# Kernel tuning notes

Measured on AMD Instinct MI355X. Metric: run time of the kernel, lower is better.

## Reference

```python
import jax, jax.numpy as jnp
import numpy as np

DIM = 1024
NUM_HEADS = 16
HEAD_DIM = DIM // NUM_HEADS
MLP_HIDDEN = 4 * DIM
TAU = 2.0
EPS = 1e-6
ALPHA_INIT = 0.01


def _xavier(key, out_f, in_f):
    limit = float(np.sqrt(6.0 / (in_f + out_f)))
    return jax.random.uniform(key, (out_f, in_f), jnp.float32, -limit, limit)


def setup_inputs() -> dict:
    key = jax.random.key(0)
    ks = jax.random.split(key, 10)
    B, Lq, Lkv = 4, 512, 2048
    return {
        "q_tokens": jax.random.normal(ks[0], (B, Lq, DIM), jnp.float32),
        "kv_tokens": jax.random.normal(ks[1], (B, Lkv, DIM), jnp.float32),
        "q_ln_w": jnp.ones((DIM,), jnp.float32),
        "q_ln_b": jnp.zeros((DIM,), jnp.float32),
        "kv_ln_w": jnp.ones((DIM,), jnp.float32),
        "kv_ln_b": jnp.zeros((DIM,), jnp.float32),
        "mlp_ln_w": jnp.ones((DIM,), jnp.float32),
        "mlp_ln_b": jnp.zeros((DIM,), jnp.float32),
        "Wq": _xavier(ks[2], DIM, DIM),
        "Wk": _xavier(ks[3], DIM, DIM),
        "Wv": _xavier(ks[4], DIM, DIM),
        "Wo": _xavier(ks[5], DIM, DIM),
        "bo": jnp.zeros((DIM,), jnp.float32),
        "fc1_w": _xavier(ks[6], MLP_HIDDEN, DIM),
        "fc1_b": jnp.zeros((MLP_HIDDEN,), jnp.float32),
        "fc2_w": _xavier(ks[7], DIM, MLP_HIDDEN),
        "fc2_b": jnp.zeros((DIM,), jnp.float32),
        "alpha_attn": jnp.full((1,), ALPHA_INIT, jnp.float32),
        "alpha_mlp": jnp.full((1,), ALPHA_INIT, jnp.float32),
    }


def _ln(x, w, b):
    mu = jnp.mean(x, axis=-1, keepdims=True)
    var = jnp.var(x, axis=-1, keepdims=True)
    return (x - mu) * jax.lax.rsqrt(var + EPS) * w + b


def _l2norm(x):
    # matches torch F.normalize: x / max(||x||, eps)
    n = jnp.sqrt(jnp.sum(x * x, axis=-1, keepdims=True))
    return x / jnp.maximum(n, EPS)


def reference(q_tokens, kv_tokens, q_ln_w, q_ln_b, kv_ln_w, kv_ln_b,
              mlp_ln_w, mlp_ln_b, Wq, Wk, Wv, Wo, bo,
              fc1_w, fc1_b, fc2_w, fc2_b, alpha_attn, alpha_mlp):
    B, Lq, D = q_tokens.shape
    q = _ln(q_tokens, q_ln_w, q_ln_b) @ Wq.T  # [B,Lq,D]
    kvn = _ln(kv_tokens, kv_ln_w, kv_ln_b)
    k = kvn @ Wk.T
    v = kvn @ Wv.T
    # split heads -> [B,H,L,hd]
    q = q.reshape(B, Lq, NUM_HEADS, HEAD_DIM)
    k = k.reshape(B, -1, NUM_HEADS, HEAD_DIM)
    v = v.reshape(B, -1, NUM_HEADS, HEAD_DIM)
    q = _l2norm(q)
    k = _l2norm(k)
    scores = jnp.einsum('bqhd,bkhd->bhqk', q, k) / TAU
    attn = jax.nn.softmax(scores, axis=-1)
    ctx = jnp.einsum('bhqk,bkhd->bqhd', attn, v).reshape(B, Lq, D)
    ctx = ctx @ Wo.T + bo
    out = q_tokens + alpha_attn * ctx
    h = _ln(out, mlp_ln_w, mlp_ln_b)
    h = jax.nn.gelu(h @ fc1_w.T + fc1_b, approximate=False)
    h = h @ fc2_w.T + fc2_b
    return out + alpha_mlp * h
```

## Files before the change

kernel.cpp:

```cpp
#include <hip/hip_runtime.h>


typedef __attribute__((ext_vector_type(8))) short short8_t;
typedef __attribute__((ext_vector_type(4))) short short4_t;
typedef __attribute__((ext_vector_type(4))) float f32x4_t;

#define WSCALE 16.0f
#define OSC (1.0f / 16.0f)

__device__ __forceinline__ float b2f(short s) {
    union { float f; unsigned u; } c;
    c.u = ((unsigned)(unsigned short)s) << 16;
    return c.f;
}
__device__ __forceinline__ short f2b(float f) {
    union { float f; unsigned u; } c;
    c.f = f;
    unsigned u = c.u;
    unsigned r = (u + 0x7FFFu + ((u >> 16) & 1u)) >> 16;
    return (short)r;
}
__device__ __forceinline__ unsigned cvt_pk_bf16(float lo, float hi) {
    unsigned r;
    asm("v_cvt_pk_bf16_f32 %0, %1, %2" : "=v"(r) : "v"(lo), "v"(hi));
    return r;
}
__device__ __forceinline__ unsigned f2f8_pk4(float a, float b, float c, float d) {
    int lo = __builtin_amdgcn_cvt_pk_fp8_f32(a, b, 0, false);
    return (unsigned)__builtin_amdgcn_cvt_pk_fp8_f32(c, d, lo, true);
}
__device__ __forceinline__ unsigned char f2f8(float a) {
    return (unsigned char)(__builtin_amdgcn_cvt_pk_fp8_f32(a, a, 0, false) & 0xff);
}

__device__ __forceinline__ void gload16(const void* g, void* l) {
    __builtin_amdgcn_global_load_lds(
        (const __attribute__((address_space(1))) void*)g,
        (__attribute__((address_space(3))) void*)l, 16, 0, 0);
}

template <int OUT8>
__device__ __forceinline__ void ln_row(
    const float* __restrict__ x, const float* __restrict__ w,
    const float* __restrict__ bia, void* __restrict__ y,
    int row, int tid, float* red)
{
    const float4 t = *(const float4*)(x + (size_t)row * 1024 + tid * 4);
    float v[4] = {t.x, t.y, t.z, t.w};
    float s = v[0] + v[1] + v[2] + v[3];
    float s2 = v[0]*v[0] + v[1]*v[1] + v[2]*v[2] + v[3]*v[3];
    #pragma unroll
    for (int off = 1; off < 64; off <<= 1) {
        s  += __shfl_xor(s, off);
        s2 += __shfl_xor(s2, off);
    }
    const int wave = tid >> 6, lane = tid & 63;
    if (lane == 0) { red[wave] = s; red[4 + wave] = s2; }
    __syncthreads();
    s  = red[0] + red[1] + red[2] + red[3];
    s2 = red[4] + red[5] + red[6] + red[7];
    const float mu  = s * (1.0f / 1024.0f);
    const float var = s2 * (1.0f / 1024.0f) - mu * mu;
    const float rstd = rsqrtf(var + 1e-6f);
    const float4 wv = *(const float4*)(w + tid * 4);
    const float4 bv = *(const float4*)(bia + tid * 4);
    const float o0 = (v[0] - mu) * rstd * wv.x + bv.x;
    const float o1 = (v[1] - mu) * rstd * wv.y + bv.y;
    const float o2 = (v[2] - mu) * rstd * wv.z + bv.z;
    const float o3 = (v[3] - mu) * rstd * wv.w + bv.w;
    if (OUT8) {
        ((unsigned*)y)[(size_t)row * 256 + tid] = f2f8_pk4(o0, o1, o2, o3);
    } else {
        short4 o;
        o.x = f2b(o0); o.y = f2b(o1); o.z = f2b(o2); o.w = f2b(o3);
        *(short4*)((short*)y + (size_t)row * 1024 + tid * 4) = o;
    }
}

__global__ __launch_bounds__(256) void prep_kernel(
    const float* __restrict__ qt, const float* __restrict__ kvt,
    const float* __restrict__ qlw, const float* __restrict__ qlb,
    const float* __restrict__ klw, const float* __restrict__ klb,
    short* __restrict__ qn, unsigned char* __restrict__ kvn8,
    const float* __restrict__ Wq, const float* __restrict__ Wo,
    const float* __restrict__ Wk, const float* __restrict__ Wv,
    const float* __restrict__ fc1w, const float* __restrict__ fc2w,
    short* __restrict__ Wq_b, short* __restrict__ Wo_b,
    unsigned char* __restrict__ Wkv8,
    unsigned char* __restrict__ fc1_8, unsigned char* __restrict__ fc2_8)
{
    __shared__ float red[8];
    const int bid = blockIdx.x, tid = threadIdx.x;
    if (bid < 2048) {
        ln_row<0>(qt, qlw, qlb, qn, bid, tid, red);
    } else if (bid < 10240) {
        ln_row<1>(kvt, klw, klb, kvn8, bid - 2048, tid, red);
    } else {
        int f = (bid - 10240) * 256 + tid;
        if (f < 524288) {
            const float* src = (f < 262144) ? Wq : Wo;
            short* dst = (f < 262144) ? Wq_b : Wo_b;
            const int off = f & 262143;
            const float4 v = ((const float4*)src)[off];
            short4 o;
            o.x = f2b(v.x); o.y = f2b(v.y); o.z = f2b(v.z); o.w = f2b(v.w);
            ((short4*)dst)[off] = o;
        } else {
            const float* src; unsigned* dst; int off;
            if (f < 1048576) {
                off = f - 524288;
                src = (off < 262144) ? Wk : Wv;
                dst = (unsigned*)Wkv8;
                if (off >= 262144) { src = Wv; }
                const int so = (off < 262144) ? off : off - 262144;
                const float4 v = ((const float4*)src)[so];
                dst[off] = f2f8_pk4(v.x * WSCALE, v.y * WSCALE,
                                    v.z * WSCALE, v.w * WSCALE);
                return;
            } else if (f < 2097152) {
                off = f - 1048576; src = fc1w; dst = (unsigned*)fc1_8;
            } else {
                off = f - 2097152; src = fc2w; dst = (unsigned*)fc2_8;
            }
            const float4 v = ((const float4*)src)[off];
            dst[off] = f2f8_pk4(v.x * WSCALE, v.y * WSCALE,
                                v.z * WSCALE, v.w * WSCALE);
        }
    }
}

__global__ __launch_bounds__(256) void ln8_kernel(
    const float* __restrict__ x, const float* __restrict__ w,
    const float* __restrict__ bia, unsigned char* __restrict__ y)
{
    __shared__ float red[8];
    ln_row<1>(x, w, bia, y, blockIdx.x, threadIdx.x, red);
}

template <int EPI, int BM>
__global__ __launch_bounds__(256) void gemm_bt_kernel(
    const short* __restrict__ A, const short* __restrict__ W,
    int M, int N, int Ks, int Kst,
    const float* __restrict__ bias,
    const float* __restrict__ resF,
    const float* __restrict__ alpha,
    short* __restrict__ out16,
    float* __restrict__ outF)
{
    constexpr int MI = (BM + 31) / 32;
    __shared__ __attribute__((aligned(16))) short As[2][BM * 64];
    __shared__ __attribute__((aligned(16))) short Bs[2][128 * 64];
    const int bm = blockIdx.y * BM, bn = blockIdx.x * 128;
    const int tid = threadIdx.x;
    const int wave = tid >> 6, lane = tid & 63;
    const int wm = (wave >> 1) * (BM / 2), wn = (wave & 1) * 64;
    const int l15 = lane & 15, quad = lane >> 4;
    const int l7 = l15 & 7;

    f32x4_t acc[MI][4];
    #pragma unroll
    for (int mi = 0; mi < MI; ++mi)
        #pragma unroll
        for (int ni = 0; ni < 4; ++ni)
            acc[mi][ni] = (f32x4_t){0.f, 0.f, 0.f, 0.f};

    auto stage = [&](int buf, int k0) {
        #pragma unroll
        for (int c = 0; c < BM / 32; ++c) {
            const int o = c * 4096 + tid * 16;
            const int row = o >> 7;
            const int g = ((o >> 4) & 7) ^ (row & 7);
            gload16(A + (size_t)(bm + row) * Kst + k0 + g * 8,
                    (char*)As[buf] + c * 4096 + wave * 1024);
        }
        #pragma unroll
        for (int c = 0; c < 4; ++c) {
            const int o = c * 4096 + tid * 16;
            const int row = o >> 7;
            const int g = ((o >> 4) & 7) ^ (row & 7);
            gload16(W + (size_t)(bn + row) * Kst + k0 + g * 8,
                    (char*)Bs[buf] + c * 4096 + wave * 1024);
        }
    };

    const int nIter = Ks >> 6;
    stage(0, 0);
    for (int it = 0; it < nIter; ++it) {
        const int buf = it & 1;
        __syncthreads();
        if (it + 1 < nIter) stage(buf ^ 1, (it + 1) * 64);
        #pragma unroll
        for (int h = 0; h < 2; ++h) {
            const int fg = (((h << 2) | quad) ^ l7) * 8;
            short8_t af[MI], bf[4];
            #pragma unroll
            for (int mi = 0; mi < MI; ++mi)
                af[mi] = *(const short8_t*)&As[buf][(wm + mi * 16 + l15) * 64 + fg];
            #pragma unroll
            for (int ni = 0; ni < 4; ++ni)
                bf[ni] = *(const short8_t*)&Bs[buf][(wn + ni * 16 + l15) * 64 + fg];
            #pragma unroll
            for (int mi = 0; mi < MI; ++mi)
                #pragma unroll
                for (int ni = 0; ni < 4; ++ni)
                    acc[mi][ni] = __builtin_amdgcn_mfma_f32_16x16x32_bf16(
                        af[mi], bf[ni], acc[mi][ni], 0, 0, 0);
        }
    }

    if (EPI == 4) {
        #pragma unroll
        for (int mi = 0; mi < MI; ++mi)
            #pragma unroll
            for (int r = 0; r < 4; ++r) {
                float s = 0.f;
                #pragma unroll
                for (int ni = 0; ni < 4; ++ni) {
                    const float x = acc[mi][ni][r];
                    s += x * x;
                }
                s += __shfl_xor(s, 1); s += __shfl_xor(s, 2);
                s += __shfl_xor(s, 4); s += __shfl_xor(s, 8);
                const float sc = 1.0f / fmaxf(sqrtf(s), 1e-6f);
                #pragma unroll
                for (int ni = 0; ni < 4; ++ni) acc[mi][ni][r] *= sc;
            }
    }

    const float a = (EPI == 1) ? alpha[0] : 0.f;
    #pragma unroll
    for (int mi = 0; mi < MI; ++mi) {
        #pragma unroll
        for (int ni = 0; ni < 4; ++ni) {
            const int n = bn + wn + ni * 16 + l15;
            const float bb = (EPI == 1) ? bias[n] : 0.f;
            #pragma unroll
            for (int r = 0; r < 4; ++r) {
                const int m = bm + wm + mi * 16 + (quad << 2) + r;
                const float x = acc[mi][ni][r];
                if (EPI == 4) {
                    out16[(size_t)m * N + n] = f2b(x);
                } else {
                    const size_t idx = (size_t)m * N + n;
                    outF[idx] = resF[idx] + a * (x + bb);
                }
            }
        }
    }
}

__device__ __forceinline__ void kvproj_body(
    unsigned char* __restrict__ pool, int bx, int by, int tid,
    const unsigned char* __restrict__ A, const unsigned char* __restrict__ W,
    short* __restrict__ khd, short* __restrict__ vhd)
{
    constexpr int BM = 128, BK = 64, MI = 4, KS = 2;
    constexpr int N = 2048, Kst = 1024;
    auto AsBuf = [&](int b) { return pool + b * (BM * BK); };
    auto BsBuf = [&](int b) { return pool + 2 * BM * BK + b * (128 * BK); };
    const int bm = by * BM, bn = bx * 128;
    const int wave = tid >> 6, lane = tid & 63;
    const int wm = (wave >> 1) * (BM / 2), wn = (wave & 1) * 64;
    const int l15 = lane & 15, quad = lane >> 4;

    f32x4_t acc[MI][4];
    #pragma unroll
    for (int mi = 0; mi < MI; ++mi)
        #pragma unroll
        for (int ni = 0; ni < 4; ++ni)
            acc[mi][ni] = (f32x4_t){0.f, 0.f, 0.f, 0.f};

    auto stage = [&](int buf, int k0) {
        #pragma unroll
        for (int c = 0; c < 2; ++c) {
            const int o = c * 4096 + tid * 16;
            const int row = o >> 6;
            const int g = ((o >> 4) & 3) ^ ((row >> 1) & 3);
            gload16(A + (size_t)(bm + row) * Kst + k0 + g * 16,
                    (char*)AsBuf(buf) + c * 4096 + wave * 1024);
        }
        #pragma unroll
        for (int c = 0; c < 2; ++c) {
            const int o = c * 4096 + tid * 16;
            const int row = o >> 6;
            const int g = ((o >> 4) & 3) ^ ((row >> 1) & 3);
            gload16(W + (size_t)(bn + row) * Kst + k0 + g * 16,
                    (char*)BsBuf(buf) + c * 4096 + wave * 1024);
        }
    };

    stage(0, 0);
    for (int it = 0; it < 16; ++it) {
        const int buf = it & 1;
        __syncthreads();
        if (it + 1 < 16) stage(buf ^ 1, (it + 1) * BK);
        #pragma unroll
        for (int ks = 0; ks < KS; ++ks) {
            const int fo = ((((ks << 1) | (quad >> 1)) ^ ((l15 >> 1) & 3)) << 4) +
                           (quad & 1) * 8;
            long af[MI], bf[4];
            #pragma unroll
            for (int mi = 0; mi < MI; ++mi)
                af[mi] = *(const long*)(AsBuf(buf) + (wm + mi * 16 + l15) * BK + fo);
            #pragma unroll
            for (int ni = 0; ni < 4; ++ni)
                bf[ni] = *(const long*)(BsBuf(buf) + (wn + ni * 16 + l15) * BK + fo);
            #pragma unroll
            for (int mi = 0; mi < MI; ++mi)
                #pragma unroll
                for (int ni = 0; ni < 4; ++ni)
                    acc[mi][ni] = __builtin_amdgcn_mfma_f32_16x16x32_fp8_fp8(
                        af[mi], bf[ni], acc[mi][ni], 0, 0, 0);
        }
    }

    const bool isK = (bn < 1024);
    if (isK) {
        #pragma unroll
        for (int mi = 0; mi < MI; ++mi)
            #pragma unroll
            for (int r = 0; r < 4; ++r) {
                float s = 0.f;
                #pragma unroll
                for (int ni = 0; ni < 4; ++ni) {
                    const float x = acc[mi][ni][r];
                    s += x * x;
                }
                s += __shfl_xor(s, 1); s += __shfl_xor(s, 2);
                s += __shfl_xor(s, 4); s += __shfl_xor(s, 8);
                const float sc = 1.0f / fmaxf(sqrtf(s), 1e-6f);
                #pragma unroll
                for (int ni = 0; ni < 4; ++ni) acc[mi][ni][r] *= sc;
            }
    }
    __syncthreads();
    short* Ct = (short*)pool;
    constexpr int LDC = 136;
    if (isK) {
        #pragma unroll
        for (int mi = 0; mi < MI; ++mi)
            #pragma unroll
            for (int ni = 0; ni < 4; ++ni) {
                const int n = wn + ni * 16 + l15;
                #pragma unroll
                for (int r = 0; r < 4; ++r)
                    Ct[(wm + mi * 16 + (quad << 2) + r) * LDC + n] =
                        f2b(acc[mi][ni][r]);
            }
    } else {
        #pragma unroll
        for (int mi = 0; mi < MI; ++mi)
            #pragma unroll
            for (int ni = 0; ni < 4; ++ni) {
                short4 pk;
                pk.x = f2b(acc[mi][ni][0] * OSC);
                pk.y = f2b(acc[mi][ni][1] * OSC);
                pk.z = f2b(acc[mi][ni][2] * OSC);
                pk.w = f2b(acc[mi][ni][3] * OSC);
                *(short4*)&Ct[(wn + ni * 16 + l15) * LDC +
                              wm + mi * 16 + (quad << 2)] = pk;
            }
    }
    __syncthreads();
    const int b_ = bm >> 11;
    const int kv0 = bm & 2047;
    #pragma unroll
    for (int p = 0; p < 8; ++p) {
        const int idx = p * 256 + tid;
        const int row = idx >> 4, ch = idx & 15;
        const short8_t v = *(const short8_t*)&Ct[row * LDC + ch * 8];
        if (isK) {
            const int hh = (bn >> 6) + (ch >> 3);
            *(short8_t*)&khd[(size_t)((b_ * 16 + hh) * 2048 + kv0 + row) * 64 +
                             (ch & 7) * 8] = v;
        } else {
            const int nn = bn - 1024 + row;
            *(short8_t*)&vhd[(size_t)((b_ * 16 + (nn >> 6)) * 64 +
                             (nn & 63)) * 2048 + kv0 + ch * 8] = v;
        }
    }
}

__device__ __forceinline__ void qproj_body(
    unsigned char* __restrict__ pool, int bx, int by, int tid,
    const short* __restrict__ A, const short* __restrict__ W,
    short* __restrict__ out16)
{
    constexpr int BM = 32, N = 1024, Kst = 1024;
    short* As = (short*)pool;
    short* Bs = (short*)(pool + 8192);
    const int bm = by * BM, bn = bx * 128;
    const int wave = tid >> 6, lane = tid & 63;
    const int wm = (wave >> 1) * 16, wn = (wave & 1) * 64;
    const int l15 = lane & 15, quad = lane >> 4;
    const int l7 = l15 & 7;

    f32x4_t acc[4];
    #pragma unroll
    for (int ni = 0; ni < 4; ++ni) acc[ni] = (f32x4_t){0.f, 0.f, 0.f, 0.f};

    auto stage = [&](int buf, int k0) {
        {
            const int o = tid * 16;
            const int row = o >> 7;
            const int g = ((o >> 4) & 7) ^ (row & 7);
            gload16(A + (size_t)(bm + row) * Kst + k0 + g * 8,
                    (char*)As + buf * 4096 + wave * 1024);
        }
        #pragma unroll
        for (int c = 0; c < 4; ++c) {
            const int o = c * 4096 + tid * 16;
            const int row = o >> 7;
            const int g = ((o >> 4) & 7) ^ (row & 7);
            gload16(W + (size_t)(bn + row) * Kst + k0 + g * 8,
                    (char*)Bs + buf * 16384 + c * 4096 + wave * 1024);
        }
    };

    stage(0, 0);
    for (int it = 0; it < 16; ++it) {
        const int buf = it & 1;
        __syncthreads();
        if (it + 1 < 16) stage(buf ^ 1, (it + 1) * 64);
        #pragma unroll
        for (int h = 0; h < 2; ++h) {
            const int fg = (((h << 2) | quad) ^ l7) * 8;
            const short8_t af =
                *(const short8_t*)&As[buf * 2048 + (wm + l15) * 64 + fg];
            short8_t bf[4];
            #pragma unroll
            for (int ni = 0; ni < 4; ++ni)
                bf[ni] = *(const short8_t*)&Bs[buf * 8192 +
                                               (wn + ni * 16 + l15) * 64 + fg];
            #pragma unroll
            for (int ni = 0; ni < 4; ++ni)
                acc[ni] = __builtin_amdgcn_mfma_f32_16x16x32_bf16(
                    af, bf[ni], acc[ni], 0, 0, 0);
        }
    }

    #pragma unroll
    for (int r = 0; r < 4; ++r) {
        float s = 0.f;
        #pragma unroll
        for (int ni = 0; ni < 4; ++ni) {
            const float x = acc[ni][r];
            s += x * x;
        }
        s += __shfl_xor(s, 1); s += __shfl_xor(s, 2);
        s += __shfl_xor(s, 4); s += __shfl_xor(s, 8);
        const float sc = 1.0f / fmaxf(sqrtf(s), 1e-6f);
        #pragma unroll
        for (int ni = 0; ni < 4; ++ni) acc[ni][r] *= sc;
    }
    #pragma unroll
    for (int ni = 0; ni < 4; ++ni) {
        const int n = bn + wn + ni * 16 + l15;
        #pragma unroll
        for (int r = 0; r < 4; ++r) {
            const int m = bm + wm + (quad << 2) + r;
            out16[(size_t)m * N + n] = f2b(acc[ni][r]);
        }
    }
}

__global__ __launch_bounds__(256, 4) void qkv_kernel(
    const unsigned char* __restrict__ kvn8, const unsigned char* __restrict__ Wkv8,
    short* __restrict__ khd, short* __restrict__ vhd,
    const short* __restrict__ qn, const short* __restrict__ Wq_b,
    short* __restrict__ qbuf)
{
    __shared__ __attribute__((aligned(16))) unsigned char pool[40960];
    const int id = blockIdx.x;
    const int xcd = id & 7, slot = id >> 3;
    const int by = xcd * 8 + (slot & 7);
    const int bx = slot >> 3;
    const int tid = threadIdx.x;
    if (bx < 16) kvproj_body(pool, bx, by, tid, kvn8, Wkv8, khd, vhd);
    else         qproj_body(pool, bx - 16, by, tid, qn, Wq_b, qbuf);
}

template <int EPI, int BM, int BK>
__global__ __launch_bounds__(256, 4) void gemm_f8_kernel(
    const unsigned char* __restrict__ A, const unsigned char* __restrict__ W,
    int M, int N, int Ks, int Kst,
    const float* __restrict__ bias,
    unsigned char* __restrict__ out8,
    short* __restrict__ out16,
    float* __restrict__ outF)
{
    constexpr int MI = BM / 32;
    constexpr int KS = BK / 32;
    constexpr int STG = 2 * BM * BK + 2 * 128 * BK;
    constexpr int EPIB = (EPI == 2) ? BM * 144 : 0;
    constexpr int POOL = (STG > EPIB) ? STG : EPIB;
    __shared__ __attribute__((aligned(16))) unsigned char pool[POOL];
    auto AsBuf = [&](int b) { return pool + b * (BM * BK); };
    auto BsBuf = [&](int b) { return pool + 2 * BM * BK + b * (128 * BK); };
    const int bm = blockIdx.y * BM, bn = blockIdx.x * 128;
    const size_t kbase = (size_t)blockIdx.z * Ks;
    const int tid = threadIdx.x;
    const int wave = tid >> 6, lane = tid & 63;
    const int wm = (wave >> 1) * (BM / 2), wn = (wave & 1) * 64;
    const int l15 = lane & 15, quad = lane >> 4;
    const int l7 = l15 & 7;

    f32x4_t acc[MI][4];
    #pragma unroll
    for (int mi = 0; mi < MI; ++mi)
        #pragma unroll
        for (int ni = 0; ni < 4; ++ni)
            acc[mi][ni] = (f32x4_t){0.f, 0.f, 0.f, 0.f};

    auto stage = [&](int buf, int k0) {
        #pragma unroll
        for (int c = 0; c < BM * BK / 4096; ++c) {
            const int o = c * 4096 + tid * 16;
            const int row = o / BK;
            int g;
            if constexpr (BK == 128) g = ((o >> 4) & 7) ^ (row & 7);
            else                     g = ((o >> 4) & 3) ^ ((row >> 1) & 3);
            gload16(A + (size_t)(bm + row) * Kst + kbase + k0 + g * 16,
                    (char*)AsBuf(buf) + c * 4096 + wave * 1024);
        }
        #pragma unroll
        for (int c = 0; c < 128 * BK / 4096; ++c) {
            const int o = c * 4096 + tid * 16;
            const int row = o / BK;
            int g;
            if constexpr (BK == 128) g = ((o >> 4) & 7) ^ (row & 7);
            else                     g = ((o >> 4) & 3) ^ ((row >> 1) & 3);
            gload16(W + (size_t)(bn + row) * Kst + kbase + k0 + g * 16,
                    (char*)BsBuf(buf) + c * 4096 + wave * 1024);
        }
    };

    const int nIter = Ks / BK;
    stage(0, 0);
    for (int it = 0; it < nIter; ++it) {
        const int buf = it & 1;
        __syncthreads();
        if (it + 1 < nIter) stage(buf ^ 1, (it + 1) * BK);
        #pragma unroll
        for (int ks = 0; ks < KS; ++ks) {
            int fo;
            if constexpr (BK == 128)
                fo = ((((ks << 1) | (quad >> 1)) ^ l7) << 4) + (quad & 1) * 8;
            else
                fo = ((((ks << 1) | (quad >> 1)) ^ ((l15 >> 1) & 3)) << 4) +
                     (quad & 1) * 8;
            long af[MI], bf[4];
            #pragma unroll
            for (int mi = 0; mi < MI; ++mi)
                af[mi] = *(const long*)(AsBuf(buf) + (wm + mi * 16 + l15) * BK + fo);
            #pragma unroll
            for (int ni = 0; ni < 4; ++ni)
                bf[ni] = *(const long*)(BsBuf(buf) + (wn + ni * 16 + l15) * BK + fo);
            #pragma unroll
            for (int mi = 0; mi < MI; ++mi)
                #pragma unroll
                for (int ni = 0; ni < 4; ++ni)
                    acc[mi][ni] = __builtin_amdgcn_mfma_f32_16x16x32_fp8_fp8(
                        af[mi], bf[ni], acc[mi][ni], 0, 0, 0);
        }
    }

    if (EPI == 2) {
        __syncthreads();
        unsigned char* C8 = (unsigned char*)pool;
        constexpr int LDC8 = 144;
        #pragma unroll
        for (int mi = 0; mi < MI; ++mi)
            #pragma unroll
            for (int ni = 0; ni < 4; ++ni) {
                const int n = wn + ni * 16 + l15;
                const float bb = bias[bn + n];
                #pragma unroll
                for (int r = 0; r < 4; ++r) {
                    const float t = acc[mi][ni][r] * OSC + bb;
                    C8[(wm + mi * 16 + (quad << 2) + r) * LDC8 + n] =
                        f2f8(0.5f * t * (1.0f + erff(t * 0.70710678118f)));
                }
            }
        __syncthreads();
        #pragma unroll
        for (int p = 0; p < MI; ++p) {
            const int idx = p * 256 + tid;
            const int row = idx >> 3, ch = idx & 7;
            const f32x4_t v = *(const f32x4_t*)&C8[row * LDC8 + ch * 16];
            *(f32x4_t*)&out8[(size_t)(bm + row) * N + bn + ch * 16] = v;
        }
        return;
    }

    #pragma unroll
    for (int mi = 0; mi < MI; ++mi) {
        #pragma unroll
        for (int ni = 0; ni < 4; ++ni) {
            const int n = bn + wn + ni * 16 + l15;
            #pragma unroll
            for (int r = 0; r < 4; ++r) {
                const int m = bm + wm + mi * 16 + (quad << 2) + r;
                out16[(size_t)blockIdx.z * M * N + (size_t)m * N + n] =
                    f2b(acc[mi][ni][r]);
            }
        }
    }
}

__global__ __launch_bounds__(256) void reduce4_kernel(
    const short* __restrict__ parts, const float* __restrict__ resF,
    const float* __restrict__ bias, const float* __restrict__ alpha,
    float* __restrict__ out)
{
    const int i = blockIdx.x * 256 + threadIdx.x;
    const size_t MN4 = (size_t)2048 * 1024 / 4;
    const float a = alpha[0];
    const float4 b4 = ((const float4*)bias)[i & 255];
    const short4 p0 = ((const short4*)parts)[i];
    const short4 p1 = ((const short4*)parts)[MN4 + i];
    const short4 p2 = ((const short4*)parts)[2 * MN4 + i];
    const short4 p3 = ((const short4*)parts)[3 * MN4 + i];
    const float4 rv = ((const float4*)resF)[i];
    float4 o;
    o.x = rv.x + a * ((b2f(p0.x) + b2f(p1.x) + b2f(p2.x) + b2f(p3.x)) * OSC + b4.x);
    o.y = rv.y + a * ((b2f(p0.y) + b2f(p1.y) + b2f(p2.y) + b2f(p3.y)) * OSC + b4.y);
    o.z = rv.z + a * ((b2f(p0.z) + b2f(p1.z) + b2f(p2.z) + b2f(p3.z)) * OSC + b4.z);
    o.w = rv.w + a * ((b2f(p0.w) + b2f(p1.w) + b2f(p2.w) + b2f(p3.w)) * OSC + b4.w);
    ((float4*)out)[i] = o;
}

__global__ __launch_bounds__(256, 4) void attn_kernel(
    const short* __restrict__ q, const short* __restrict__ khd,
    const short* __restrict__ vhd, short* __restrict__ o0,
    short* __restrict__ o1, float* __restrict__ lpart)
{
    const int h  = blockIdx.x;
    const int b  = blockIdx.y;
    const int qt = blockIdx.z >> 1;
    const int sp = blockIdx.z & 1;
    const int tid = threadIdx.x;
    const int wave = tid >> 6, lane = tid & 63;
    const int l15 = lane & 15, quad = lane >> 4;
    const int q0 = qt * 64 + wave * 16;
    const int t0 = sp * 16;

    __shared__ __attribute__((aligned(16))) short Ks[2][4096];
    __shared__ __attribute__((aligned(16))) short Vs[2][4096];

    const short* qbase = q + (size_t)(b * 512 + q0 + l15) * 1024 + h * 64 + quad * 8;
    const short8_t aq0 = *(const short8_t*)(qbase);
    const short8_t aq1 = *(const short8_t*)(qbase + 32);

    const short* kbase = khd + (size_t)(b * 16 + h) * 2048 * 64;
    const short* vbase = vhd + (size_t)(b * 16 + h) * 64 * 2048;

    const int swz = l15 & 7;
    const int g0 = (quad ^ swz) * 8;
    const int g1 = ((quad ^ swz) ^ 4) * 8;

    auto stage = [&](int buf, int t) {
        #pragma unroll
        for (int c = 0; c < 2; ++c) {
            const int o = c * 4096 + tid * 16;
            const int row = o >> 7;
            const int g = ((o >> 4) & 7) ^ (row & 7);
            gload16(kbase + (size_t)(t * 64 + row) * 64 + g * 8,
                    (char*)Ks[buf] + c * 4096 + wave * 1024);
            gload16(vbase + (size_t)row * 2048 + t * 64 + g * 8,
                    (char*)Vs[buf] + c * 4096 + wave * 1024);
        }
    };

    const short4_t ones4 = {(short)0x3F80, (short)0x3F80,
                            (short)0x3F80, (short)0x3F80};

    f32x4_t oacc[4];
    #pragma unroll
    for (int u = 0; u < 4; ++u) oacc[u] = (f32x4_t){0.f, 0.f, 0.f, 0.f};
    f32x4_t lacc = (f32x4_t){0.f, 0.f, 0.f, 0.f};

    stage(0, t0);
    for (int tt = 0; tt < 16; ++tt) {
        const int buf = tt & 1;
        __syncthreads();
        if (tt + 1 < 16) stage(buf ^ 1, t0 + tt + 1);

        f32x4_t s[4];
        __builtin_amdgcn_s_setprio(1);
        #pragma unroll
        for (int ss = 0; ss < 4; ++ss) {
            const int R = ss * 16 + l15;
            const short8_t bk0 = *(const short8_t*)&Ks[buf][R * 64 + g0];
            const short8_t bk1 = *(const short8_t*)&Ks[buf][R * 64 + g1];
            f32x4_t a = (f32x4_t){0.f, 0.f, 0.f, 0.f};
            a = __builtin_amdgcn_mfma_f32_16x16x32_bf16(bk0, aq0, a, 0, 0, 0);
            a = __builtin_amdgcn_mfma_f32_16x16x32_bf16(bk1, aq1, a, 0, 0, 0);
            s[ss] = a;
        }
        __builtin_amdgcn_s_setprio(0);
        short4_t pa[4];
        #pragma unroll
        for (int ss = 0; ss < 4; ++ss) {
            const float p0 = __expf(s[ss][0] * 0.5f);
            const float p1 = __expf(s[ss][1] * 0.5f);
            const float p2 = __expf(s[ss][2] * 0.5f);
            const float p3 = __expf(s[ss][3] * 0.5f);
            union { unsigned w[2]; short4_t v; } u_;
            u_.w[0] = cvt_pk_bf16(p0, p1);
            u_.w[1] = cvt_pk_bf16(p2, p3);
            pa[ss] = u_.v;
        }
        __builtin_amdgcn_s_setprio(1);
        #pragma unroll
        for (int ss = 0; ss < 4; ++ss)
            lacc = __builtin_amdgcn_mfma_f32_16x16x16bf16_1k(
                pa[ss], ones4, lacc, 0, 0, 0);
        #pragma unroll
        for (int ss = 0; ss < 4; ++ss) {
            const int ch = (((ss * 2 + (quad >> 1)) ^ swz) << 3) + ((quad & 1) << 2);
            #pragma unroll
            for (int u = 0; u < 4; ++u) {
                const short4_t bv =
                    *(const short4_t*)&Vs[buf][(u * 16 + l15) * 64 + ch];
                oacc[u] = __builtin_amdgcn_mfma_f32_16x16x16bf16_1k(
                    pa[ss], bv, oacc[u], 0, 0, 0);
            }
        }
        __builtin_amdgcn_s_setprio(0);
    }

    short* ob = sp ? o1 : o0;
    float* lb = lpart + (size_t)sp * 2048 * 16;
    #pragma unroll
    for (int u = 0; u < 4; ++u)
        #pragma unroll
        for (int r = 0; r < 4; ++r)
            ob[(size_t)(b * 512 + q0 + quad * 4 + r) * 1024 + h * 64 + u * 16 + l15] =
                f2b(oacc[u][r]);
    if (l15 == 0) {
        #pragma unroll
        for (int r = 0; r < 4; ++r)
            lb[(size_t)(b * 512 + q0 + quad * 4 + r) * 16 + h] = lacc[r];
    }
}

__global__ __launch_bounds__(256) void attn_combine_kernel(
    const short* __restrict__ o0, const short* __restrict__ o1,
    const float* __restrict__ lpart, short* __restrict__ ctx)
{
    const int i = blockIdx.x * 256 + threadIdx.x;
    const int row = i >> 8;
    const int h = (i & 255) >> 4;
    const float l = lpart[row * 16 + h] + lpart[2048 * 16 + row * 16 + h];
    const float inv = 1.0f / l;
    const short4 a4 = ((const short4*)o0)[i];
    const short4 c4 = ((const short4*)o1)[i];
    short4 o;
    o.x = f2b((b2f(a4.x) + b2f(c4.x)) * inv);
    o.y = f2b((b2f(a4.y) + b2f(c4.y)) * inv);
    o.z = f2b((b2f(a4.z) + b2f(c4.z)) * inv);
    o.w = f2b((b2f(a4.w) + b2f(c4.w)) * inv);
    ((short4*)ctx)[i] = o;
}

extern "C" void kernel_launch(void* const* d_in, const int* in_sizes, int n_in,
                              void* d_out, int out_size, void* d_ws, size_t ws_size,
                              hipStream_t stream)
{
    const float* q_tokens  = (const float*)d_in[0];
    const float* kv_tokens = (const float*)d_in[1];
    const float* q_ln_w    = (const float*)d_in[2];
    const float* q_ln_b    = (const float*)d_in[3];
    const float* kv_ln_w   = (const float*)d_in[4];
    const float* kv_ln_b   = (const float*)d_in[5];
    const float* mlp_ln_w  = (const float*)d_in[6];
    const float* mlp_ln_b  = (const float*)d_in[7];
    const float* Wq        = (const float*)d_in[8];
    const float* Wk        = (const float*)d_in[9];
    const float* Wv        = (const float*)d_in[10];
    const float* Wo        = (const float*)d_in[11];
    const float* bo        = (const float*)d_in[12];
    const float* fc1_w     = (const float*)d_in[13];
    const float* fc1_b     = (const float*)d_in[14];
    const float* fc2_w     = (const float*)d_in[15];
    const float* fc2_b     = (const float*)d_in[16];
    const float* alpha_attn = (const float*)d_in[17];
    const float* alpha_mlp  = (const float*)d_in[18];

    char* ws = (char*)d_ws;
    const size_t MB = (size_t)1 << 20;
    short* khd    = (short*)(ws);
    short* vhd    = (short*)(ws + 16 * MB);
    short* parts  = (short*)(ws);
    unsigned char* kvn8 = (unsigned char*)(ws + 32 * MB);
    short* attn_o0 = (short*)(ws + 32 * MB);
    unsigned char* h1   = (unsigned char*)(ws + 32 * MB);
    short* qn     = (short*)(ws + 40 * MB);
    short* qbuf   = (short*)(ws + 44 * MB);
    short* ctx    = (short*)(ws + 48 * MB);
    float* aout   = (float*)(ws + 52 * MB);
    short* attn_o1 = (short*)(ws + 52 * MB);
    unsigned char* hn8 = (unsigned char*)(ws + 60 * MB);
    float* attn_l  = (float*)(ws + 60 * MB);
    short* Wq_b   = (short*)(ws + 62 * MB);
    short* Wo_b   = (short*)(ws + 64 * MB);
    unsigned char* Wkv8  = (unsigned char*)(ws + 66 * MB);
    unsigned char* fc1_8 = (unsigned char*)(ws + 68 * MB);
    unsigned char* fc2_8 = (unsigned char*)(ws + 72 * MB);

    prep_kernel<<<22528, 256, 0, stream>>>(
        q_tokens, kv_tokens, q_ln_w, q_ln_b, kv_ln_w, kv_ln_b, qn, kvn8,
        Wq, Wo, Wk, Wv, fc1_w, fc2_w,
        Wq_b, Wo_b, Wkv8, fc1_8, fc2_8);

    qkv_kernel<<<1536, 256, 0, stream>>>(
        kvn8, Wkv8, khd, vhd, qn, Wq_b, qbuf);

    attn_kernel<<<dim3(16, 4, 16), 256, 0, stream>>>(
        qbuf, khd, vhd, attn_o0, attn_o1, attn_l);
    attn_combine_kernel<<<2048, 256, 0, stream>>>(attn_o0, attn_o1, attn_l, ctx);

    gemm_bt_kernel<1, 32><<<dim3(8, 64), 256, 0, stream>>>(
        ctx, Wo_b, 2048, 1024, 1024, 1024, bo, q_tokens, alpha_attn, nullptr, aout);

    ln8_kernel<<<2048, 256, 0, stream>>>(aout, mlp_ln_w, mlp_ln_b, hn8);

    gemm_f8_kernel<2, 64, 64><<<dim3(32, 32), 256, 0, stream>>>(
        hn8, fc1_8, 2048, 4096, 1024, 1024, fc1_b, h1, nullptr, nullptr);

    gemm_f8_kernel<7, 64, 64><<<dim3(8, 32, 4), 256, 0, stream>>>(
        h1, fc2_8, 2048, 1024, 1024, 4096, nullptr, nullptr, parts, nullptr);
    reduce4_kernel<<<2048, 256, 0, stream>>>(parts, aout, fc2_b, alpha_mlp,
                                             (float*)d_out);
}
```

Before: 282.4 us.

## Switch FP8 GEMMs to MI355 scaled 16x16x128 MFMA with BK=128 tiles

```diff
diff --git a/kernel.cpp b/kernel.cpp
--- a/kernel.cpp
+++ b/kernel.cpp
@@ -4,9 +4,12 @@
 typedef __attribute__((ext_vector_type(8))) short short8_t;
 typedef __attribute__((ext_vector_type(4))) short short4_t;
 typedef __attribute__((ext_vector_type(4))) float f32x4_t;
+typedef __attribute__((ext_vector_type(8))) int int8v_t;
+typedef __attribute__((ext_vector_type(4))) int int4v_t;
 
 #define WSCALE 16.0f
 #define OSC (1.0f / 16.0f)
+#define SCL1 127
 
 __device__ __forceinline__ float b2f(short s) {
     union { float f; unsigned u; } c;
@@ -37,6 +40,15 @@
     __builtin_amdgcn_global_load_lds(
         (const __attribute__((address_space(1))) void*)g,
         (__attribute__((address_space(3))) void*)l, 16, 0, 0);
+}
+
+__device__ __forceinline__ int8v_t ld32(const unsigned char* base, int g0, int g1) {
+    const int4v_t lo = *(const int4v_t*)(base + g0);
+    const int4v_t hi = *(const int4v_t*)(base + g1);
+    int8v_t r;
+    r[0] = lo[0]; r[1] = lo[1]; r[2] = lo[2]; r[3] = lo[3];
+    r[4] = hi[0]; r[5] = hi[1]; r[6] = hi[2]; r[7] = hi[3];
+    return r;
 }
 
 template <int OUT8>
@@ -254,14 +266,15 @@
     const unsigned char* __restrict__ A, const unsigned char* __restrict__ W,
     short* __restrict__ khd, short* __restrict__ vhd)
 {
-    constexpr int BM = 128, BK = 64, MI = 4, KS = 2;
-    constexpr int N = 2048, Kst = 1024;
+    constexpr int BM = 128, BK = 128, MI = 4;
+    constexpr int Kst = 1024;
     auto AsBuf = [&](int b) { return pool + b * (BM * BK); };
     auto BsBuf = [&](int b) { return pool + 2 * BM * BK + b * (128 * BK); };
     const int bm = by * BM, bn = bx * 128;
     const int wave = tid >> 6, lane = tid & 63;
     const int wm = (wave >> 1) * (BM / 2), wn = (wave & 1) * 64;
     const int l15 = lane & 15, quad = lane >> 4;
+    const int l7 = l15 & 7;
 
     f32x4_t acc[MI][4];
     #pragma unroll
@@ -272,46 +285,44 @@
 
     auto stage = [&](int buf, int k0) {
         #pragma unroll
-        for (int c = 0; c < 2; ++c) {
+        for (int c = 0; c < 4; ++c) {
             const int o = c * 4096 + tid * 16;
-            const int row = o >> 6;
-            const int g = ((o >> 4) & 3) ^ ((row >> 1) & 3);
+            const int row = o >> 7;
+            const int g = ((o >> 4) & 7) ^ (row & 7);
             gload16(A + (size_t)(bm + row) * Kst + k0 + g * 16,
                     (char*)AsBuf(buf) + c * 4096 + wave * 1024);
         }
         #pragma unroll
-        for (int c = 0; c < 2; ++c) {
+        for (int c = 0; c < 4; ++c) {
             const int o = c * 4096 + tid * 16;
-            const int row = o >> 6;
-            const int g = ((o >> 4) & 3) ^ ((row >> 1) & 3);
+            const int row = o >> 7;
+            const int g = ((o >> 4) & 7) ^ (row & 7);
             gload16(W + (size_t)(bn + row) * Kst + k0 + g * 16,
                     (char*)BsBuf(buf) + c * 4096 + wave * 1024);
         }
     };
 
+    const int ga = ((quad << 1) ^ l7) << 4;
+    const int gb = (((quad << 1) | 1) ^ l7) << 4;
+
     stage(0, 0);
-    for (int it = 0; it < 16; ++it) {
+    for (int it = 0; it < 8; ++it) {
         const int buf = it & 1;
         __syncthreads();
-        if (it + 1 < 16) stage(buf ^ 1, (it + 1) * BK);
-        #pragma unroll
-        for (int ks = 0; ks < KS; ++ks) {
-            const int fo = ((((ks << 1) | (quad >> 1)) ^ ((l15 >> 1) & 3)) << 4) +
-                           (quad & 1) * 8;
-            long af[MI], bf[4];
-            #pragma unroll
-            for (int mi = 0; mi < MI; ++mi)
-                af[mi] = *(const long*)(AsBuf(buf) + (wm + mi * 16 + l15) * BK + fo);
+        if (it + 1 < 8) stage(buf ^ 1, (it + 1) * BK);
+        int8v_t af[MI], bf[4];
+        #pragma unroll
+        for (int mi = 0; mi < MI; ++mi)
+            af[mi] = ld32(AsBuf(buf) + (wm + mi * 16 + l15) * BK, ga, gb);
+        #pragma unroll
+        for (int ni = 0; ni < 4; ++ni)
+            bf[ni] = ld32(BsBuf(buf) + (wn + ni * 16 + l15) * BK, ga, gb);
+        #pragma unroll
+        for (int mi = 0; mi < MI; ++mi)
             #pragma unroll
             for (int ni = 0; ni < 4; ++ni)
-                bf[ni] = *(const long*)(BsBuf(buf) + (wn + ni * 16 + l15) * BK + fo);
-            #pragma unroll
-            for (int mi = 0; mi < MI; ++mi)
-                #pragma unroll
-                for (int ni = 0; ni < 4; ++ni)
-                    acc[mi][ni] = __builtin_amdgcn_mfma_f32_16x16x32_fp8_fp8(
-                        af[mi], bf[ni], acc[mi][ni], 0, 0, 0);
-        }
+                acc[mi][ni] = __builtin_amdgcn_mfma_scale_f32_16x16x128_f8f6f4(
+                    af[mi], bf[ni], acc[mi][ni], 0, 0, 0, SCL1, 0, SCL1);
     }
 
     const bool isK = (bn < 1024);
@@ -464,13 +475,13 @@
     }
 }
 
-__global__ __launch_bounds__(256, 4) void qkv_kernel(
+__global__ __launch_bounds__(256, 2) void qkv_kernel(
     const unsigned char* __restrict__ kvn8, const unsigned char* __restrict__ Wkv8,
     short* __restrict__ khd, short* __restrict__ vhd,
     const short* __restrict__ qn, const short* __restrict__ Wq_b,
     short* __restrict__ qbuf)
 {
-    __shared__ __attribute__((aligned(16))) unsigned char pool[40960];
+    __shared__ __attribute__((aligned(16))) unsigned char pool[65536];
     const int id = blockIdx.x;
     const int xcd = id & 7, slot = id >> 3;
     const int by = xcd * 8 + (slot & 7);
@@ -480,8 +491,8 @@
     else         qproj_body(pool, bx - 16, by, tid, qn, Wq_b, qbuf);
 }
 
-template <int EPI, int BM, int BK>
-__global__ __launch_bounds__(256, 4) void gemm_f8_kernel(
+template <int EPI, int BM>
+__global__ __launch_bounds__(256, 2) void gemm_f8_kernel(
     const unsigned char* __restrict__ A, const unsigned char* __restrict__ W,
     int M, int N, int Ks, int Kst,
     const float* __restrict__ bias,
@@ -490,7 +501,7 @@
     float* __restrict__ outF)
 {
     constexpr int MI = BM / 32;
-    constexpr int KS = BK / 32;
+    constexpr int BK = 128;
     constexpr int STG = 2 * BM * BK + 2 * 128 * BK;
     constexpr int EPIB = (EPI == 2) ? BM * 144 : 0;
     constexpr int POOL = (STG > EPIB) ? STG : EPIB;
@@ -516,53 +527,43 @@
         #pragma unroll
         for (int c = 0; c < BM * BK / 4096; ++c) {
             const int o = c * 4096 + tid * 16;
-            const int row = o / BK;
-            int g;
-            if constexpr (BK == 128) g = ((o >> 4) & 7) ^ (row & 7);
-            else                     g = ((o >> 4) & 3) ^ ((row >> 1) & 3);
+            const int row = o >> 7;
+            const int g = ((o >> 4) & 7) ^ (row & 7);
             gload16(A + (size_t)(bm + row) * Kst + kbase + k0 + g * 16,
                     (char*)AsBuf(buf) + c * 4096 + wave * 1024);
         }
         #pragma unroll
-        for (int c = 0; c < 128 * BK / 4096; ++c) {
+        for (int c = 0; c < 4; ++c) {
             const int o = c * 4096 + tid * 16;
-            const int row = o / BK;
-            int g;
-            if constexpr (BK == 128) g = ((o >> 4) & 7) ^ (row & 7);
-            else                     g = ((o >> 4) & 3) ^ ((row >> 1) & 3);
+            const int row = o >> 7;
+            const int g = ((o >> 4) & 7) ^ (row & 7);
             gload16(W + (size_t)(bn + row) * Kst + kbase + k0 + g * 16,
                     (char*)BsBuf(buf) + c * 4096 + wave * 1024);
         }
     };
 
-    const int nIter = Ks / BK;
+    const int ga = ((quad << 1) ^ l7) << 4;
+    const int gb = (((quad << 1) | 1) ^ l7) << 4;
+
+    const int nIter = Ks >> 7;
     stage(0, 0);
     for (int it = 0; it < nIter; ++it) {
         const int buf = it & 1;
         __syncthreads();
         if (it + 1 < nIter) stage(buf ^ 1, (it + 1) * BK);
-        #pragma unroll
-        for (int ks = 0; ks < KS; ++ks) {
-            int fo;
-            if constexpr (BK == 128)
-                fo = ((((ks << 1) | (quad >> 1)) ^ l7) << 4) + (quad & 1) * 8;
-            else
-                fo = ((((ks << 1) | (quad >> 1)) ^ ((l15 >> 1) & 3)) << 4) +
-                     (quad & 1) * 8;
-            long af[MI], bf[4];
-            #pragma unroll
-            for (int mi = 0; mi < MI; ++mi)
-                af[mi] = *(const long*)(AsBuf(buf) + (wm + mi * 16 + l15) * BK + fo);
+        int8v_t af[MI], bf[4];
+        #pragma unroll
+        for (int mi = 0; mi < MI; ++mi)
+            af[mi] = ld32(AsBuf(buf) + (wm + mi * 16 + l15) * BK, ga, gb);
+        #pragma unroll
+        for (int ni = 0; ni < 4; ++ni)
+            bf[ni] = ld32(BsBuf(buf) + (wn + ni * 16 + l15) * BK, ga, gb);
+        #pragma unroll
+        for (int mi = 0; mi < MI; ++mi)
             #pragma unroll
             for (int ni = 0; ni < 4; ++ni)
-                bf[ni] = *(const long*)(BsBuf(buf) + (wn + ni * 16 + l15) * BK + fo);
-            #pragma unroll
-            for (int mi = 0; mi < MI; ++mi)
-                #pragma unroll
-                for (int ni = 0; ni < 4; ++ni)
-                    acc[mi][ni] = __builtin_amdgcn_mfma_f32_16x16x32_fp8_fp8(
-                        af[mi], bf[ni], acc[mi][ni], 0, 0, 0);
-        }
+                acc[mi][ni] = __builtin_amdgcn_mfma_scale_f32_16x16x128_f8f6f4(
+                    af[mi], bf[ni], acc[mi][ni], 0, 0, 0, SCL1, 0, SCL1);
     }
 
     if (EPI == 2) {
@@ -826,10 +827,10 @@
 
     ln8_kernel<<<2048, 256, 0, stream>>>(aout, mlp_ln_w, mlp_ln_b, hn8);
 
-    gemm_f8_kernel<2, 64, 64><<<dim3(32, 32), 256, 0, stream>>>(
+    gemm_f8_kernel<2, 64><<<dim3(32, 32), 256, 0, stream>>>(
         hn8, fc1_8, 2048, 4096, 1024, 1024, fc1_b, h1, nullptr, nullptr);
 
-    gemm_f8_kernel<7, 64, 64><<<dim3(8, 32, 4), 256, 0, stream>>>(
+    gemm_f8_kernel<7, 64><<<dim3(8, 32, 4), 256, 0, stream>>>(
         h1, fc2_8, 2048, 1024, 1024, 4096, nullptr, nullptr, parts, nullptr);
     reduce4_kernel<<<2048, 256, 0, stream>>>(parts, aout, fc2_b, alpha_mlp,
                                              (float*)d_out);
```

Result: slower. 289.7 us (+2.6%).
